# Optimization experiments

Hardware: AMD Instinct MI355X
Metric: run time of the kernel (lower is better)

The kernel has to match this reference:

```python
import jax, jax.numpy as jnp
import numpy as np
import math

TSCALE, DSCALE = 128, 128
NUM_SAMPLE, NSPB, EXT = 32, 3, 0.5
C_IN, C_HID, C_ROI, C_OUT = 256, 128, 512, 128
BATCH = 2


def _interp1d_bin_mask(seg_xmin, seg_xmax, tscale, num_sample, nspb):
    plen = float(seg_xmax - seg_xmin)
    plen_sample = plen / (num_sample * nspb - 1.0)
    samples = [seg_xmin + plen_sample * ii for ii in range(num_sample * nspb)]
    p_mask = np.zeros([tscale, num_sample])
    for idx in range(num_sample):
        for s in samples[idx * nspb:(idx + 1) * nspb]:
            s_up = math.ceil(s)
            s_dec, s_dn = math.modf(s)
            if 0 <= int(s_dn) <= tscale - 1:
                p_mask[int(s_dn), idx] += 1 - s_dec
            if 0 <= int(s_up) <= tscale - 1:
                p_mask[int(s_up), idx] += s_dec
    return p_mask / nspb


def _build_sample_mask(tscale, dscale, num_sample, nspb, ext):
    mask_mat = []
    for start in range(tscale):
        col = []
        for dur in range(dscale):
            if start + dur < tscale:
                p_xmin, p_xmax = start, start + dur
                clen = float(p_xmax - p_xmin) + 1
                col.append(_interp1d_bin_mask(p_xmin - clen * ext, p_xmax + clen * ext,
                                              tscale, num_sample, nspb))
            else:
                col.append(np.zeros([tscale, num_sample]))
        mask_mat.append(np.stack(col, axis=2))  # [T, N, D]
    return np.stack(mask_mat, axis=3).astype(np.float32)  # [T, N, D, Tout]


def setup_inputs() -> dict:
    key = jax.random.key(0)
    ks = jax.random.split(key, 7)
    x = jax.random.normal(ks[0], (BATCH, C_IN, TSCALE), dtype=jnp.float32)
    w_red = jax.random.normal(ks[1], (C_HID, C_IN, 3), dtype=jnp.float32) * 0.05
    b_red = jax.random.normal(ks[2], (C_HID,), dtype=jnp.float32) * 0.05
    w3d = jax.random.normal(ks[3], (C_ROI, C_HID, NUM_SAMPLE), dtype=jnp.float32) * 0.05
    b3d = jax.random.normal(ks[4], (C_ROI,), dtype=jnp.float32) * 0.05
    w2d = jax.random.normal(ks[5], (C_OUT, C_ROI), dtype=jnp.float32) * 0.05
    b2d = jax.random.normal(ks[6], (C_OUT,), dtype=jnp.float32) * 0.05
    sample_mask = jnp.asarray(_build_sample_mask(TSCALE, DSCALE, NUM_SAMPLE, NSPB, EXT))
    return {"x": x, "w_red": w_red, "b_red": b_red, "w3d": w3d, "b3d": b3d,
            "w2d": w2d, "b2d": b2d, "sample_mask": sample_mask}


def reference(x, w_red, b_red, w3d, b3d, w2d, b2d, sample_mask):
    # Conv1d(256->128, k=3, pad=1) + ReLU
    h = jax.lax.conv_general_dilated(x, w_red, window_strides=(1,), padding='SAME',
                                     dimension_numbers=('NCH', 'OIH', 'NCH'))
    h = jax.nn.relu(h + b_red[None, :, None])  # [B, C_HID, T]
    # Boundary-matching tensordot: [B,C,T] x [T,N,D,Tout] -> [B,C,N,D,Tout]
    map_base = jnp.einsum('bct,tndm->bcndm', h, sample_mask)
    # Conv2d((32,1) stride (32,1)) == contraction over (C, N) per (d, t) cell
    m3 = jax.nn.relu(jnp.einsum('ocn,bcndm->bodm', w3d, map_base)
                     + b3d[None, :, None, None])  # [B, C_ROI, D, Tout]
    # 1x1 Conv2d + ReLU
    out = jax.nn.relu(jnp.einsum('oc,bcdm->bodm', w2d, m3)
                      + b2d[None, :, None, None])  # [B, C_OUT, D, Tout]
    return out
```

## Files before the change

### kernel.cpp

```cpp
#include <hip/hip_runtime.h>

typedef unsigned short u16;
typedef unsigned int u32;
typedef unsigned long long u64;
typedef _Float16 f16x8 __attribute__((ext_vector_type(8)));
typedef float f32x4 __attribute__((ext_vector_type(4)));

__device__ __forceinline__ u16 f2h(float f) {
    _Float16 h = (_Float16)f;
    return __builtin_bit_cast(u16, h);
}

__global__ void setup_kernel(const float* __restrict__ x, const float* __restrict__ w_red,
                             const float* __restrict__ b_red, const float* __restrict__ w3d,
                             const float* __restrict__ w2d, const float* __restrict__ b3,
                             const float* __restrict__ b2,
                             u16* __restrict__ W3n, u16* __restrict__ hT16,
                             u16* __restrict__ W2h, int* __restrict__ tab,
                             float* __restrict__ c0,
                             int* __restrict__ tapT0, u16* __restrict__ tapW) {
#pragma clang fp contract(off)
    int bid = blockIdx.x, tid = threadIdx.x;
    if (bid < 256) {
        int oc = bid * 256 + tid;
        float4 v[8];
        const float4* src = (const float4*)(w3d + (size_t)oc * 32);
#pragma unroll
        for (int j = 0; j < 8; ++j) v[j] = src[j];
        const float* vf = (const float*)v;
#pragma unroll
        for (int n = 0; n < 32; ++n)
            W3n[n * 65536 + oc] = f2h(vf[n]);
        return;
    }
    if (bid < 512) {
        if (tid >= 128) return;
        int idx = bid - 256;
        int co = idx & 127, b = idx >> 7, t = tid;
        float acc = b_red[co];
        const float* xb = x + b * 256 * 128;
        const float* wr = w_red + co * 768;
        for (int ci = 0; ci < 256; ++ci) {
            float w0 = wr[ci * 3 + 0], w1 = wr[ci * 3 + 1], w2 = wr[ci * 3 + 2];
            float x1 = xb[ci * 128 + t];
            float x0 = (t >= 1)   ? xb[ci * 128 + t - 1] : 0.f;
            float x2 = (t < 127) ? xb[ci * 128 + t + 1] : 0.f;
            acc += x0 * w0 + x1 * w1 + x2 * w2;
        }
        hT16[b * 16384 + t * 128 + co] = f2h(fmaxf(acc, 0.f));
        return;
    }
    if (bid < 768) {
        int i = (bid - 512) * 256 + tid;
        W2h[i] = f2h(w2d[i]);
        return;
    }
    if (bid < 1800) {
        int gid = (bid - 768) * 256 + tid;
        int n = gid / 8256, cell = gid - n * 8256;
        int off = 0, d = 0;
        while (d < 128) { int w = 128 - d; if (cell < off + w) break; off += w; ++d; }
        int m = cell - off;
        double xm = m - (d + 1) * 0.5;
        double step = (2 * d + 1) / 95.0;
        int t0 = (int)floor(xm + step * (double)(3 * n));
        int dnr[3], upr[3]; double av[3], bv[3];
#pragma unroll
        for (int j = 0; j < 3; ++j) {
            double p = step * (double)(3 * n + j);
            double s = xm + p;
            double tr = trunc(s);
            double dec = s - tr;
            int dn = (int)tr, up = (int)ceil(s);
            dnr[j] = dn - t0; upr[j] = up - t0;
            av[j] = (dn >= 0 && dn <= 127) ? (1.0 - dec) * (1.0 / 3.0) : 0.0;
            bv[j] = (up >= 0 && up <= 127) ? dec * (1.0 / 3.0) : 0.0;
        }
#pragma unroll
        for (int sl = 0; sl < 8; ++sl) {
            double a = 0.0;
#pragma unroll
            for (int j = 0; j < 3; ++j) {
                a += (dnr[j] == sl) ? av[j] : 0.0;
                a += (upr[j] == sl) ? bv[j] : 0.0;
            }
            tapW[(size_t)gid * 8 + sl] = f2h((float)a);
        }
        tapT0[gid] = t0;
        return;
    }
    if (bid == 1800) {
        for (int cell = tid; cell < 8256; cell += 256) {
            int off = 0, d = 0;
            while (d < 128) { int w = 128 - d; if (cell < off + w) break; off += w; ++d; }
            tab[cell] = (d << 8) | (cell - off);
        }
        return;
    }
    int o2 = tid >> 1, half = tid & 1;
    float s = 0.f;
    const float* row = w2d + o2 * 512 + half * 256;
    for (int o = 0; o < 256; ++o) s += row[o] * fmaxf(b3[half * 256 + o], 0.f);
    s += __shfl_xor(s, 1);
    if (half == 0) c0[o2] = fmaxf(s + b2[o2], 0.f);
}

__global__ __launch_bounds__(256) void smd_build(const int* __restrict__ tapT0,
                                                 const u16* __restrict__ tapW,
                                                 u16* __restrict__ SMd) {
    __shared__ alignas(16) u16 rows[4][4096];
    const int tid = threadIdx.x;
    const int cid = tid >> 6, l = tid & 63;
    const int cell = blockIdx.x * 4 + cid;
    char* rowb = (char*)&rows[cid][0];
    f32x4 z = {0.f, 0.f, 0.f, 0.f};
#pragma unroll
    for (int j = 0; j < 8; ++j)
        *(f32x4*)(rowb + l * 128 + j * 16) = z;
    __syncthreads();
    if (l < 32) {
        int e = l * 8256 + cell;
        int t0 = tapT0[e];
        const u64* wp = (const u64*)(tapW + (size_t)e * 8);
        u64 w01 = wp[0], w23 = wp[1];
#pragma unroll
        for (int k = 0; k < 8; ++k) {
            int t = t0 + k;
            if ((unsigned)t < 128u)
                rows[cid][l * 128 + t] = (u16)(((k < 4) ? w01 : w23) >> (16 * (k & 3)));
        }
    }
    __syncthreads();
    u16* dst = SMd + (size_t)cell * 4096;
#pragma unroll
    for (int j = 0; j < 8; ++j)
        *(f32x4*)((char*)dst + l * 16 + j * 1024) = *(const f32x4*)(rowb + l * 16 + j * 1024);
}

__global__ __launch_bounds__(256) void gkern(const u16* __restrict__ W3n,
                                             const u16* __restrict__ hT16,
                                             u16* __restrict__ G) {
    __shared__ alignas(16) u16 As[128 * 128];
    __shared__ alignas(16) u16 Bs[128 * 128];
    const int tid = threadIdx.x;
    const int lane = tid & 63, wv = tid >> 6;
    const int fr = lane & 15, fq = lane >> 4;
    const int bid = blockIdx.x;
    const int b = bid & 1, n = (bid >> 1) & 31, os = bid >> 6;
    const u16* Abase = W3n + n * 65536 + os * 128 * 128;
    const u16* Bbase = hT16 + b * 16384;
#pragma unroll
    for (int i = 0; i < 8; ++i) {
        int off = i * 4096 + tid * 16;
        int row = off >> 8, colb = off & 255;
        int scol = colb ^ ((row & 7) << 4);
        __builtin_amdgcn_global_load_lds(
            (const __attribute__((address_space(1))) void*)(Abase + row * 128 + (scol >> 1)),
            (__attribute__((address_space(3))) void*)((char*)As + off), 16, 0, 0);
        __builtin_amdgcn_global_load_lds(
            (const __attribute__((address_space(1))) void*)(Bbase + row * 128 + (scol >> 1)),
            (__attribute__((address_space(3))) void*)((char*)Bs + off), 16, 0, 0);
    }
    asm volatile("s_waitcnt vmcnt(0)" ::: "memory");
    __syncthreads();
    const int wm = wv >> 1, wn = wv & 1;
    f32x4 acc[4][4] = {};
#pragma unroll
    for (int kk = 0; kk < 4; ++kk) {
        int kb = kk * 64 + fq * 16;
        f16x8 af[4], bf[4];
#pragma unroll
        for (int mf = 0; mf < 4; ++mf) {
            int row = wm * 64 + mf * 16 + fr;
            af[mf] = *(const f16x8*)((const char*)As + row * 256 + (kb ^ ((row & 7) << 4)));
        }
#pragma unroll
        for (int nf = 0; nf < 4; ++nf) {
            int row = wn * 64 + nf * 16 + fr;
            bf[nf] = *(const f16x8*)((const char*)Bs + row * 256 + (kb ^ ((row & 7) << 4)));
        }
#pragma unroll
        for (int mf = 0; mf < 4; ++mf)
#pragma unroll
            for (int nf = 0; nf < 4; ++nf)
                acc[mf][nf] = __builtin_amdgcn_mfma_f32_16x16x32_f16(
                    af[mf], bf[nf], acc[mf][nf], 0, 0, 0);
    }
    u16* Gb = G + (size_t)b * 2097152;
#pragma unroll
    for (int mf = 0; mf < 4; ++mf) {
        int o = os * 128 + wm * 64 + mf * 16 + (fq << 2);
#pragma unroll
        for (int nf = 0; nf < 4; ++nf) {
            int t = wn * 64 + nf * 16 + fr;
            f32x4 v = acc[mf][nf];
#pragma unroll
            for (int r = 0; r < 4; ++r)
                Gb[(size_t)(o + r) * 4096 + n * 128 + t] = f2h(v[r]);
        }
    }
}

__global__ __launch_bounds__(256, 2) void mega_kernel(
        const u16* __restrict__ G, const u16* __restrict__ SMd,
        const float* __restrict__ b3, u16* __restrict__ m3T) {
    __shared__ alignas(16) char lds[73728];

    const int tid = threadIdx.x;
    const int lane = tid & 63, wv = tid >> 6;
    const int fr = lane & 15, fq = lane >> 4;
    const int swz = (fr & 7) << 4;
    const int wm = wv >> 1, wn = wv & 1;

    const int id = blockIdx.x;
    const int p = (id >> 6) * 8 + (id & 7);
    const int s = (id >> 3) & 7;
    if (p > 128) return;
    const int cell0 = p * 64;
    const int m0 = s * 128;

    f32x4 acc[4][2] = {};

    auto stage = [&](int buf, int kt) {
        char* A = lds + buf * 16384;
        char* B = lds + 49152 + buf * 8192;
#pragma unroll
        for (int i2 = 0; i2 < 4; ++i2) {
            int off = i2 * 4096 + tid * 16;
            int row = off >> 7, colb = off & 127;
            int scol = colb ^ ((row & 7) << 4);
            const u16* ga = G + (size_t)(m0 + row) * 4096 + kt + (scol >> 1);
            __builtin_amdgcn_global_load_lds(
                (const __attribute__((address_space(1))) void*)ga,
                (__attribute__((address_space(3))) void*)(A + off), 16, 0, 0);
        }
#pragma unroll
        for (int i2 = 0; i2 < 2; ++i2) {
            int off = i2 * 4096 + tid * 16;
            int row = off >> 7, colb = off & 127;
            int scol = colb ^ ((row & 7) << 4);
            const u16* gb = SMd + (size_t)(cell0 + row) * 4096 + kt + (scol >> 1);
            __builtin_amdgcn_global_load_lds(
                (const __attribute__((address_space(1))) void*)gb,
                (__attribute__((address_space(3))) void*)(B + off), 16, 0, 0);
        }
    };

    stage(0, 0);
    stage(1, 64);
    asm volatile("s_waitcnt vmcnt(6)" ::: "memory");
    __builtin_amdgcn_sched_barrier(0);
    __builtin_amdgcn_s_barrier();
    __builtin_amdgcn_sched_barrier(0);

    int cur = 0;
    for (int t64 = 0; t64 < 64; ++t64) {
        const char* A = lds + cur * 16384;
        const char* Bp = lds + 49152 + cur * 8192;
#pragma unroll
        for (int kk = 0; kk < 2; ++kk) {
            const int kb = (kk * 64 + (fq << 4)) ^ swz;
            f16x8 af[4], bfr[2];
#pragma unroll
            for (int mf = 0; mf < 4; ++mf)
                af[mf] = *(const f16x8*)(A + (wm * 64 + mf * 16 + fr) * 128 + kb);
#pragma unroll
            for (int nf = 0; nf < 2; ++nf)
                bfr[nf] = *(const f16x8*)(Bp + (wn * 32 + nf * 16 + fr) * 128 + kb);
            __builtin_amdgcn_s_setprio(1);
#pragma unroll
            for (int mf = 0; mf < 4; ++mf)
#pragma unroll
                for (int nf = 0; nf < 2; ++nf)
                    acc[mf][nf] = __builtin_amdgcn_mfma_f32_16x16x32_f16(
                        af[mf], bfr[nf], acc[mf][nf], 0, 0, 0);
            __builtin_amdgcn_s_setprio(0);
        }
        int nxt = cur + 2; if (nxt >= 3) nxt -= 3;
        if (t64 < 62) {
            stage(nxt, (t64 + 2) << 6);
            asm volatile("s_waitcnt vmcnt(6)" ::: "memory");
        } else {
            asm volatile("s_waitcnt vmcnt(0)" ::: "memory");
        }
        __builtin_amdgcn_sched_barrier(0);
        __builtin_amdgcn_s_barrier();
        __builtin_amdgcn_sched_barrier(0);
        cur += 1; if (cur >= 3) cur -= 3;
    }

#pragma unroll
    for (int mf = 0; mf < 4; ++mf) {
        int m = m0 + wm * 64 + mf * 16 + (fq << 2);
        int b = m >> 9, o = m & 511;
#pragma unroll
        for (int nf = 0; nf < 2; ++nf) {
            int cl = wn * 32 + nf * 16 + fr;
            f32x4 v = acc[mf][nf];
            u64 pw = 0;
#pragma unroll
            for (int r = 0; r < 4; ++r) {
                float z = fmaxf(v[r] + b3[o + r], 0.f);
                pw |= (u64)f2h(z) << (16 * r);
            }
            *(u64*)(m3T + ((size_t)(b * 8256 + cell0 + cl)) * 512 + o) = pw;
        }
    }
}

__global__ __launch_bounds__(256, 2) void gemm2f_kernel(const u16* __restrict__ A,
                                                        const u16* __restrict__ B,
                                                        const float* __restrict__ bias,
                                                        const int* __restrict__ tab,
                                                        const float* __restrict__ c0,
                                                        float* __restrict__ out) {
    __shared__ alignas(16) char lds[73728];
    if (blockIdx.x >= 258) {
        int idx = blockIdx.x - 258;
        int d = idx & 127, b = idx >> 7;
        if (d == 0) return;
        int cnt = d, total = 128 * cnt;
        for (int j = threadIdx.x; j < total; j += blockDim.x) {
            int o2 = j / cnt, m = 128 - cnt + (j % cnt);
            out[((size_t)b << 21) + ((size_t)o2 << 14) + (d << 7) + m] = c0[o2];
        }
        return;
    }
    const int tid = threadIdx.x;
    const int lane = tid & 63, wave = tid >> 6;
    const int m0 = blockIdx.x * 64;
    const int wr = wave & 1, wc = wave >> 1;
    const int fr = lane & 15, fq = lane >> 4;
    const int swz = (fr & 7) << 4;
    f32x4 acc[2][4] = {};

    auto stage = [&](int buf, int kt) {
        char* As = lds + buf * 8192;
        char* Bs = lds + 24576 + buf * 16384;
#pragma unroll
        for (int i = 0; i < 2; ++i) {
            int off = i * 4096 + tid * 16;
            int row = off >> 7, colb = off & 127;
            int scol = colb ^ ((row & 7) << 4);
            const u16* ga = A + (size_t)(m0 + row) * 512 + kt + (scol >> 1);
            __builtin_amdgcn_global_load_lds(
                (const __attribute__((address_space(1))) void*)ga,
                (__attribute__((address_space(3))) void*)(As + off), 16, 0, 0);
        }
#pragma unroll
        for (int i = 0; i < 4; ++i) {
            int off = i * 4096 + tid * 16;
            int row = off >> 7, colb = off & 127;
            int scol = colb ^ ((row & 7) << 4);
            const u16* gb = B + (size_t)row * 512 + kt + (scol >> 1);
            __builtin_amdgcn_global_load_lds(
                (const __attribute__((address_space(1))) void*)gb,
                (__attribute__((address_space(3))) void*)(Bs + off), 16, 0, 0);
        }
    };

    stage(0, 0);
    stage(1, 64);
    asm volatile("s_waitcnt vmcnt(6)" ::: "memory");
    __builtin_amdgcn_sched_barrier(0);
    __builtin_amdgcn_s_barrier();
    __builtin_amdgcn_sched_barrier(0);

    int cur = 0;
    for (int t = 0; t < 8; ++t) {
        const char* As = lds + cur * 8192;
        const char* Bs = lds + 24576 + cur * 16384;
#pragma unroll
        for (int kk = 0; kk < 2; ++kk) {
            const int kb = (kk * 64 + (fq << 4)) ^ swz;
            f16x8 af[2], bfr[4];
#pragma unroll
            for (int mf = 0; mf < 2; ++mf)
                af[mf] = *(const f16x8*)(As + (wr * 32 + mf * 16 + fr) * 128 + kb);
#pragma unroll
            for (int nf = 0; nf < 4; ++nf)
                bfr[nf] = *(const f16x8*)(Bs + (wc * 64 + nf * 16 + fr) * 128 + kb);
#pragma unroll
            for (int mf = 0; mf < 2; ++mf)
#pragma unroll
                for (int nf = 0; nf < 4; ++nf)
                    acc[mf][nf] = __builtin_amdgcn_mfma_f32_16x16x32_f16(
                        af[mf], bfr[nf], acc[mf][nf], 0, 0, 0);
        }
        int nxt = cur + 2; if (nxt >= 3) nxt -= 3;
        if (t < 6) {
            stage(nxt, (t + 2) << 6);
            asm volatile("s_waitcnt vmcnt(6)" ::: "memory");
        } else {
            asm volatile("s_waitcnt vmcnt(0)" ::: "memory");
        }
        __builtin_amdgcn_sched_barrier(0);
        __builtin_amdgcn_s_barrier();
        __builtin_amdgcn_sched_barrier(0);
        cur += 1; if (cur >= 3) cur -= 3;
    }

#pragma unroll
    for (int mf = 0; mf < 2; ++mf) {
        int rbase = m0 + wr * 32 + mf * 16 + (fq << 2);
#pragma unroll
        for (int nf = 0; nf < 4; ++nf) {
            int o2 = wc * 64 + nf * 16 + fr;
            f32x4 v = acc[mf][nf];
#pragma unroll
            for (int r = 0; r < 4; ++r) {
                int colg = rbase + r;
                int b = (colg >= 8256) ? 1 : 0;
                int cell = colg - b * 8256;
                int dm = tab[cell];
                float z = fmaxf(v[r] + bias[o2], 0.f);
                out[((size_t)b << 21) + ((size_t)o2 << 14) + ((dm >> 8) << 7) + (dm & 255)] = z;
            }
        }
    }
}

extern "C" void kernel_launch(void* const* d_in, const int* in_sizes, int n_in,
                              void* d_out, int out_size, void* d_ws, size_t ws_size,
                              hipStream_t stream) {
    const float* x     = (const float*)d_in[0];
    const float* w_red = (const float*)d_in[1];
    const float* b_red = (const float*)d_in[2];
    const float* w3d   = (const float*)d_in[3];
    const float* b3d   = (const float*)d_in[4];
    const float* w2d   = (const float*)d_in[5];
    const float* b2d   = (const float*)d_in[6];
    float* out = (float*)d_out;

    char* ws = (char*)d_ws;
    u16*   hT16  = (u16*)(ws + 0);
    u16*   W3n   = (u16*)(ws + 65536);
    u16*   W2h   = (u16*)(ws + 4259840);
    float* c0    = (float*)(ws + 4390912);
    int*   tab   = (int*)(ws + 4391424);
    int*   tapT0 = (int*)(ws + 4457472);
    u16*   tapW  = (u16*)(ws + 5514240);
    u16*   G     = (u16*)(ws + 9741312);
    u16*   m3T   = (u16*)(ws + 18129920);
    u16*   SMd   = (u16*)(ws + 35038208);

    setup_kernel<<<1802, 256, 0, stream>>>(x, w_red, b_red, w3d, w2d, b3d, b2d,
                                           W3n, hT16, W2h, tab, c0, tapT0, tapW);
    smd_build<<<2064, 256, 0, stream>>>(tapT0, tapW, SMd);
    gkern<<<256, 256, 0, stream>>>(W3n, hT16, G);
    mega_kernel<<<1088, 256, 0, stream>>>(G, SMd, b3d, m3T);
    gemm2f_kernel<<<514, 256, 0, stream>>>(m3T, W2h, b2d, tab, c0, out);
}
```

Baseline: 198.1 us.

## Fuse sample-mask build into setup kernel and widen mega_kernel N tile to 128

The sample-mask tap computation and the SMd row scatter move into the setup kernel, so the separate smd_build launch and the tapT0/tapW round trip through global memory go away. mega_kernel now tiles 128 cells per block instead of 64, with a 4x4 MFMA accumulator per wave. The B operand uses its own double buffer loaded one step ahead, while A keeps its triple buffer. One tail block covers the last 64 cells, which reduces the grid and the reloads of the G operand, at the cost of more LDS (80KB) and more accumulator registers, which may lower occupancy.

After: 175.3 us. -11.5%, faster.

```diff
diff --git a/kernel.cpp b/kernel.cpp
--- a/kernel.cpp
+++ b/kernel.cpp
@@ -11,15 +11,16 @@
     return __builtin_bit_cast(u16, h);
 }
 
-__global__ void setup_kernel(const float* __restrict__ x, const float* __restrict__ w_red,
-                             const float* __restrict__ b_red, const float* __restrict__ w3d,
-                             const float* __restrict__ w2d, const float* __restrict__ b3,
-                             const float* __restrict__ b2,
-                             u16* __restrict__ W3n, u16* __restrict__ hT16,
-                             u16* __restrict__ W2h, int* __restrict__ tab,
-                             float* __restrict__ c0,
-                             int* __restrict__ tapT0, u16* __restrict__ tapW) {
+__global__ __launch_bounds__(256) void setup_kernel(
+        const float* __restrict__ x, const float* __restrict__ w_red,
+        const float* __restrict__ b_red, const float* __restrict__ w3d,
+        const float* __restrict__ w2d, const float* __restrict__ b3,
+        const float* __restrict__ b2,
+        u16* __restrict__ W3n, u16* __restrict__ hT16,
+        u16* __restrict__ W2h, int* __restrict__ tab,
+        float* __restrict__ c0, u16* __restrict__ SMd) {
 #pragma clang fp contract(off)
+    __shared__ alignas(16) u16 rows[4][4096];
     int bid = blockIdx.x, tid = threadIdx.x;
     if (bid < 256) {
         int oc = bid * 256 + tid;
@@ -55,9 +56,33 @@
         W2h[i] = f2h(w2d[i]);
         return;
     }
-    if (bid < 1800) {
-        int gid = (bid - 768) * 256 + tid;
-        int n = gid / 8256, cell = gid - n * 8256;
+    if (bid == 768) {
+        for (int cell = tid; cell < 8256; cell += 256) {
+            int off = 0, d = 0;
+            while (d < 128) { int w = 128 - d; if (cell < off + w) break; off += w; ++d; }
+            tab[cell] = (d << 8) | (cell - off);
+        }
+        return;
+    }
+    if (bid == 769) {
+        int o2 = tid >> 1, half = tid & 1;
+        float s = 0.f;
+        const float* row = w2d + o2 * 512 + half * 256;
+        for (int o = 0; o < 256; ++o) s += row[o] * fmaxf(b3[half * 256 + o], 0.f);
+        s += __shfl_xor(s, 1);
+        if (half == 0) c0[o2] = fmaxf(s + b2[o2], 0.f);
+        return;
+    }
+    const int cid = tid >> 6, l = tid & 63;
+    const int cell = (bid - 770) * 4 + cid;
+    char* rowb = (char*)&rows[cid][0];
+    f32x4 z = {0.f, 0.f, 0.f, 0.f};
+#pragma unroll
+    for (int j = 0; j < 8; ++j)
+        *(f32x4*)(rowb + l * 128 + j * 16) = z;
+    __syncthreads();
+    if (l < 32) {
+        int n = l;
         int off = 0, d = 0;
         while (d < 128) { int w = 128 - d; if (cell < off + w) break; off += w; ++d; }
         int m = cell - off;
@@ -84,50 +109,9 @@
                 a += (dnr[j] == sl) ? av[j] : 0.0;
                 a += (upr[j] == sl) ? bv[j] : 0.0;
             }
-            tapW[(size_t)gid * 8 + sl] = f2h((float)a);
-        }
-        tapT0[gid] = t0;
-        return;
-    }
-    if (bid == 1800) {
-        for (int cell = tid; cell < 8256; cell += 256) {
-            int off = 0, d = 0;
-            while (d < 128) { int w = 128 - d; if (cell < off + w) break; off += w; ++d; }
-            tab[cell] = (d << 8) | (cell - off);
-        }
-        return;
-    }
-    int o2 = tid >> 1, half = tid & 1;
-    float s = 0.f;
-    const float* row = w2d + o2 * 512 + half * 256;
-    for (int o = 0; o < 256; ++o) s += row[o] * fmaxf(b3[half * 256 + o], 0.f);
-    s += __shfl_xor(s, 1);
-    if (half == 0) c0[o2] = fmaxf(s + b2[o2], 0.f);
-}
-
-__global__ __launch_bounds__(256) void smd_build(const int* __restrict__ tapT0,
-                                                 const u16* __restrict__ tapW,
-                                                 u16* __restrict__ SMd) {
-    __shared__ alignas(16) u16 rows[4][4096];
-    const int tid = threadIdx.x;
-    const int cid = tid >> 6, l = tid & 63;
-    const int cell = blockIdx.x * 4 + cid;
-    char* rowb = (char*)&rows[cid][0];
-    f32x4 z = {0.f, 0.f, 0.f, 0.f};
-#pragma unroll
-    for (int j = 0; j < 8; ++j)
-        *(f32x4*)(rowb + l * 128 + j * 16) = z;
-    __syncthreads();
-    if (l < 32) {
-        int e = l * 8256 + cell;
-        int t0 = tapT0[e];
-        const u64* wp = (const u64*)(tapW + (size_t)e * 8);
-        u64 w01 = wp[0], w23 = wp[1];
-#pragma unroll
-        for (int k = 0; k < 8; ++k) {
-            int t = t0 + k;
+            int t = t0 + sl;
             if ((unsigned)t < 128u)
-                rows[cid][l * 128 + t] = (u16)(((k < 4) ? w01 : w23) >> (16 * (k & 3)));
+                rows[cid][n * 128 + t] = f2h((float)a);
         }
     }
     __syncthreads();
@@ -204,7 +188,7 @@
 __global__ __launch_bounds__(256, 2) void mega_kernel(
         const u16* __restrict__ G, const u16* __restrict__ SMd,
         const float* __restrict__ b3, u16* __restrict__ m3T) {
-    __shared__ alignas(16) char lds[73728];
+    __shared__ alignas(16) char lds[81920];
 
     const int tid = threadIdx.x;
     const int lane = tid & 63, wv = tid >> 6;
@@ -213,17 +197,17 @@
     const int wm = wv >> 1, wn = wv & 1;
 
     const int id = blockIdx.x;
-    const int p = (id >> 6) * 8 + (id & 7);
-    const int s = (id >> 3) & 7;
-    if (p > 128) return;
-    const int cell0 = p * 64;
+    int p, s;
+    if (id < 512) { int c = id >> 6, r = id & 63; p = c * 8 + (r & 7); s = r >> 3; }
+    else          { p = 64; s = id - 512; }
+    const int cell0 = p * 128;
+    const int cn = (p == 64) ? 64 : 128;
     const int m0 = s * 128;
 
-    f32x4 acc[4][2] = {};
-
-    auto stage = [&](int buf, int kt) {
+    f32x4 acc[4][4] = {};
+
+    auto stageA = [&](int buf, int kt) {
         char* A = lds + buf * 16384;
-        char* B = lds + 49152 + buf * 8192;
 #pragma unroll
         for (int i2 = 0; i2 < 4; ++i2) {
             int off = i2 * 4096 + tid * 16;
@@ -234,52 +218,58 @@
                 (const __attribute__((address_space(1))) void*)ga,
                 (__attribute__((address_space(3))) void*)(A + off), 16, 0, 0);
         }
-#pragma unroll
-        for (int i2 = 0; i2 < 2; ++i2) {
+    };
+    auto stageB = [&](int buf, int kt) {
+        char* B = lds + 49152 + buf * 16384;
+#pragma unroll
+        for (int i2 = 0; i2 < 4; ++i2) {
             int off = i2 * 4096 + tid * 16;
             int row = off >> 7, colb = off & 127;
+            int r2 = row < cn ? row : 0;
             int scol = colb ^ ((row & 7) << 4);
-            const u16* gb = SMd + (size_t)(cell0 + row) * 4096 + kt + (scol >> 1);
+            const u16* gb = SMd + (size_t)(cell0 + r2) * 4096 + kt + (scol >> 1);
             __builtin_amdgcn_global_load_lds(
                 (const __attribute__((address_space(1))) void*)gb,
                 (__attribute__((address_space(3))) void*)(B + off), 16, 0, 0);
         }
     };
 
-    stage(0, 0);
-    stage(1, 64);
-    asm volatile("s_waitcnt vmcnt(6)" ::: "memory");
+    stageB(0, 0);
+    stageA(0, 0);
+    stageA(1, 64);
+    asm volatile("s_waitcnt vmcnt(4)" ::: "memory");
     __builtin_amdgcn_sched_barrier(0);
     __builtin_amdgcn_s_barrier();
     __builtin_amdgcn_sched_barrier(0);
 
     int cur = 0;
-    for (int t64 = 0; t64 < 64; ++t64) {
+    for (int t = 0; t < 64; ++t) {
+        if (t < 63) stageB((t + 1) & 1, (t + 1) << 6);
         const char* A = lds + cur * 16384;
-        const char* Bp = lds + 49152 + cur * 8192;
+        const char* Bp = lds + 49152 + (t & 1) * 16384;
 #pragma unroll
         for (int kk = 0; kk < 2; ++kk) {
             const int kb = (kk * 64 + (fq << 4)) ^ swz;
-            f16x8 af[4], bfr[2];
+            f16x8 af[4], bfr[4];
 #pragma unroll
             for (int mf = 0; mf < 4; ++mf)
                 af[mf] = *(const f16x8*)(A + (wm * 64 + mf * 16 + fr) * 128 + kb);
 #pragma unroll
-            for (int nf = 0; nf < 2; ++nf)
-                bfr[nf] = *(const f16x8*)(Bp + (wn * 32 + nf * 16 + fr) * 128 + kb);
+            for (int nf = 0; nf < 4; ++nf)
+                bfr[nf] = *(const f16x8*)(Bp + (wn * 64 + nf * 16 + fr) * 128 + kb);
             __builtin_amdgcn_s_setprio(1);
 #pragma unroll
             for (int mf = 0; mf < 4; ++mf)
 #pragma unroll
-                for (int nf = 0; nf < 2; ++nf)
+                for (int nf = 0; nf < 4; ++nf)
                     acc[mf][nf] = __builtin_amdgcn_mfma_f32_16x16x32_f16(
                         af[mf], bfr[nf], acc[mf][nf], 0, 0, 0);
             __builtin_amdgcn_s_setprio(0);
         }
         int nxt = cur + 2; if (nxt >= 3) nxt -= 3;
-        if (t64 < 62) {
-            stage(nxt, (t64 + 2) << 6);
-            asm volatile("s_waitcnt vmcnt(6)" ::: "memory");
+        if (t < 62) {
+            stageA(nxt, (t + 2) << 6);
+            asm volatile("s_waitcnt vmcnt(4)" ::: "memory");
         } else {
             asm volatile("s_waitcnt vmcnt(0)" ::: "memory");
         }
@@ -294,16 +284,18 @@
         int m = m0 + wm * 64 + mf * 16 + (fq << 2);
         int b = m >> 9, o = m & 511;
 #pragma unroll
-        for (int nf = 0; nf < 2; ++nf) {
-            int cl = wn * 32 + nf * 16 + fr;
-            f32x4 v = acc[mf][nf];
-            u64 pw = 0;
-#pragma unroll
-            for (int r = 0; r < 4; ++r) {
-                float z = fmaxf(v[r] + b3[o + r], 0.f);
-                pw |= (u64)f2h(z) << (16 * r);
+        for (int nf = 0; nf < 4; ++nf) {
+            int cl = wn * 64 + nf * 16 + fr;
+            if (cl < cn) {
+                f32x4 v = acc[mf][nf];
+                u64 pw = 0;
+#pragma unroll
+                for (int r = 0; r < 4; ++r) {
+                    float z = fmaxf(v[r] + b3[o + r], 0.f);
+                    pw |= (u64)f2h(z) << (16 * r);
+                }
+                *(u64*)(m3T + ((size_t)(b * 8256 + cell0 + cl)) * 512 + o) = pw;
             }
-            *(u64*)(m3T + ((size_t)(b * 8256 + cell0 + cl)) * 512 + o) = pw;
         }
     }
 }
@@ -438,16 +430,13 @@
     u16*   W2h   = (u16*)(ws + 4259840);
     float* c0    = (float*)(ws + 4390912);
     int*   tab   = (int*)(ws + 4391424);
-    int*   tapT0 = (int*)(ws + 4457472);
-    u16*   tapW  = (u16*)(ws + 5514240);
     u16*   G     = (u16*)(ws + 9741312);
     u16*   m3T   = (u16*)(ws + 18129920);
     u16*   SMd   = (u16*)(ws + 35038208);
 
-    setup_kernel<<<1802, 256, 0, stream>>>(x, w_red, b_red, w3d, w2d, b3d, b2d,
-                                           W3n, hT16, W2h, tab, c0, tapT0, tapW);
-    smd_build<<<2064, 256, 0, stream>>>(tapT0, tapW, SMd);
+    setup_kernel<<<2834, 256, 0, stream>>>(x, w_red, b_red, w3d, w2d, b3d, b2d,
+                                           W3n, hT16, W2h, tab, c0, SMd);
     gkern<<<256, 256, 0, stream>>>(W3n, hT16, G);
-    mega_kernel<<<1088, 256, 0, stream>>>(G, SMd, b3d, m3T);
+    mega_kernel<<<520, 256, 0, stream>>>(G, SMd, b3d, m3T);
     gemm2f_kernel<<<514, 256, 0, stream>>>(m3T, W2h, b2d, tab, c0, out);
 }
```
